# Optimization experiments

Measured on AMD Instinct MI355X. Metric: run time of the kernel, lower is better.

The kernel has to match this reference:

```python
import jax, jax.numpy as jnp
import numpy as np

DIM = 96
DIM_OUT = 96
NUM_HEADS = 1
HEAD_DIM = DIM_OUT // NUM_HEADS  # 96, also depthwise-conv channel count
STRIDE_Q = 1
STRIDE_KV = 2
EPS = 1e-6


def _layernorm(t, g, b):
    mu = jnp.mean(t, axis=-1, keepdims=True)
    var = jnp.mean(jnp.square(t - mu), axis=-1, keepdims=True)
    return (t - mu) * jax.lax.rsqrt(var + EPS) * g + b


def _depthwise(t_nchw, w, stride):
    # torch Conv2d(C, C, 3, stride, padding=1, groups=C, bias=False)
    # w: [C, 1, 3, 3]
    return jax.lax.conv_general_dilated(
        t_nchw, w, window_strides=(stride, stride), padding=[(1, 1), (1, 1)],
        feature_group_count=HEAD_DIM, dimension_numbers=('NCHW', 'OIHW', 'NCHW'))


def _attention_pool(t, w, stride, g, b, H, W):
    # t: [B, heads, L, C] -> pooled [B, heads, Lp, C]
    B, nh, L, C = t.shape
    t = t.reshape(B * nh, H, W, C).transpose(0, 3, 1, 2)  # [B*nh, C, H, W]
    t = _depthwise(t, w, stride)
    Hp, Wp = t.shape[2], t.shape[3]
    t = t.reshape(B, nh, C, Hp * Wp).transpose(0, 1, 3, 2)  # [B, nh, Lp, C]
    return _layernorm(t, g, b), Hp, Wp


def setup_inputs() -> dict:
    key = jax.random.key(0)
    ks = jax.random.split(key, 16)
    B, N = 32, 56 * 56
    inp = {
        'x': jax.random.normal(ks[0], (B, N, DIM), dtype=jnp.float32),
        'Wqkv': jax.random.normal(ks[1], (3 * DIM_OUT, DIM), dtype=jnp.float32) * 0.02,
        'bqkv': jax.random.normal(ks[2], (3 * DIM_OUT,), dtype=jnp.float32) * 0.02,
        'pool_q_w': jax.random.normal(ks[3], (HEAD_DIM, 1, 3, 3), dtype=jnp.float32) * 0.1,
        'gq': 1.0 + jax.random.normal(ks[4], (HEAD_DIM,), dtype=jnp.float32) * 0.02,
        'betq': jax.random.normal(ks[5], (HEAD_DIM,), dtype=jnp.float32) * 0.02,
        'pool_k_w': jax.random.normal(ks[6], (HEAD_DIM, 1, 3, 3), dtype=jnp.float32) * 0.1,
        'gk': 1.0 + jax.random.normal(ks[7], (HEAD_DIM,), dtype=jnp.float32) * 0.02,
        'betk': jax.random.normal(ks[8], (HEAD_DIM,), dtype=jnp.float32) * 0.02,
        'pool_v_w': jax.random.normal(ks[9], (HEAD_DIM, 1, 3, 3), dtype=jnp.float32) * 0.1,
        'gv': 1.0 + jax.random.normal(ks[10], (HEAD_DIM,), dtype=jnp.float32) * 0.02,
        'betv': jax.random.normal(ks[11], (HEAD_DIM,), dtype=jnp.float32) * 0.02,
        'Wproj': jax.random.normal(ks[12], (DIM_OUT, DIM_OUT), dtype=jnp.float32) * 0.02,
        'bproj': jax.random.normal(ks[13], (DIM_OUT,), dtype=jnp.float32) * 0.02,
        'h': 56,
        'w': 56,
    }
    return inp


def reference(x, Wqkv, bqkv, pool_q_w, gq, betq, pool_k_w, gk, betk,
              pool_v_w, gv, betv, Wproj, bproj, h, w):
    B, N, _ = x.shape
    qkv = (jnp.einsum('bnd,ed->bne', x, Wqkv) + bqkv)
    qkv = qkv.reshape(B, N, 3, NUM_HEADS, HEAD_DIM).transpose(2, 0, 3, 1, 4)
    q, k, v = qkv[0], qkv[1], qkv[2]  # each [B, heads, N, head_dim]

    q, Hq, Wq = _attention_pool(q, pool_q_w, STRIDE_Q, gq, betq, h, w)
    k, _, _ = _attention_pool(k, pool_k_w, STRIDE_KV, gk, betk, h, w)
    v, _, _ = _attention_pool(v, pool_v_w, STRIDE_KV, gv, betv, h, w)

    scale = HEAD_DIM ** -0.5
    attn = jax.nn.softmax(jnp.einsum('bhqc,bhkc->bhqk', q * scale, k), axis=-1)
    out = jnp.einsum('bhqk,bhkc->bhqc', attn, v) + q  # residual x + q
    out = out.transpose(0, 2, 1, 3).reshape(B, Hq * Wq, DIM_OUT)
    out = jnp.einsum('bnd,ed->bne', out, Wproj) + bproj
    return out
```

## Files before the change

kernel.cpp:

```cpp
#include <hip/hip_runtime.h>
#include <hip/hip_bf16.h>
#include <cmath>

#define BATCH 32
#define H_IN 56
#define W_IN 56
#define N_IN (H_IN * W_IN)
#define LKV 784
#define LKV_PAD 864
#define FRAG_ELEMS 82944

typedef short bf16x8 __attribute__((ext_vector_type(8)));
typedef float f32x4 __attribute__((ext_vector_type(4)));
typedef float f32x16 __attribute__((ext_vector_type(16)));

__device__ __forceinline__ unsigned pack_bf16(float a, float b) {
    unsigned ua = __builtin_bit_cast(unsigned, a);
    unsigned ub = __builtin_bit_cast(unsigned, b);
    ua = (ua + 0x7FFFu + ((ua >> 16) & 1u)) >> 16;
    ub = (ub + 0x7FFFu + ((ub >> 16) & 1u)) >> 16;
    return ua | (ub << 16);
}

__device__ __forceinline__ unsigned short cvt_bf16(float a) {
    unsigned ua = __builtin_bit_cast(unsigned, a);
    return (unsigned short)((ua + 0x7FFFu + ((ua >> 16) & 1u)) >> 16);
}

__device__ __forceinline__ float bf16_to_f32(unsigned short u) {
    unsigned v = ((unsigned)u) << 16;
    return __builtin_bit_cast(float, v);
}

__device__ __forceinline__ float bflo(unsigned u) {
    return __builtin_bit_cast(float, u << 16);
}
__device__ __forceinline__ float bfhi(unsigned u) {
    return __builtin_bit_cast(float, u & 0xFFFF0000u);
}

__device__ __forceinline__ unsigned pack_trunc(float a, float b) {
    return __builtin_amdgcn_perm(__builtin_bit_cast(unsigned, b),
                                 __builtin_bit_cast(unsigned, a), 0x07060302u);
}

__device__ __forceinline__ f32x16 zero16() {
    f32x16 z;
#pragma unroll
    for (int i = 0; i < 16; ++i) z[i] = 0.f;
    return z;
}

__global__ __launch_bounds__(256) void wprep_kernel(
    const float* __restrict__ Wqkv, const float* __restrict__ Wproj,
    const float* __restrict__ pqw, const float* __restrict__ pkw,
    const float* __restrict__ pvw,
    unsigned short* __restrict__ wq, unsigned short* __restrict__ wp,
    float* __restrict__ wpool)
{
    int idx = blockIdx.x * 256 + threadIdx.x;
    if (idx < 4608) {
        const float* src; unsigned short* dst; int li;
        if (idx < 3456) { src = Wqkv; dst = wq; li = idx; }
        else            { src = Wproj; dst = wp; li = idx - 3456; }
        int frag = li >> 6, ln = li & 63;
        int ct = frag / 3, kkb = frag % 3;
        int ch = ct * 16 + (ln & 15);
        int k0 = kkb * 32 + (ln >> 4) * 8;
        const float* s = src + ch * 96 + k0;
        float4 v0 = *reinterpret_cast<const float4*>(s);
        float4 v1 = *reinterpret_cast<const float4*>(s + 4);
        uint4 o;
        o.x = pack_bf16(v0.x, v0.y); o.y = pack_bf16(v0.z, v0.w);
        o.z = pack_bf16(v1.x, v1.y); o.w = pack_bf16(v1.z, v1.w);
        *reinterpret_cast<uint4*>(dst + (size_t)li * 8) = o;
    } else if (idx < 7200) {
        int li = idx - 4608;
        int which = li / 864, r = li % 864;
        int tap = r / 96, c = r % 96;
        const float* src = (which == 0) ? pqw : (which == 1 ? pkw : pvw);
        wpool[which * 864 + tap * 96 + c] = src[c * 9 + tap];
    }
}

template <int NCT, bool IN_BF16, bool OUT_F32>
__global__ __launch_bounds__(256, 2) void gemm2_kernel(
    const void* __restrict__ Xv, const unsigned short* __restrict__ Wfr,
    const float* __restrict__ bias, void* __restrict__ o0,
    void* __restrict__ o1, void* __restrict__ o2)
{
    __shared__ unsigned short Wl[NCT * 192 * 8];
    const int tid = threadIdx.x;
    const int wid = tid >> 6, lane = tid & 63;
    const int lo16 = lane & 15, hi = lane >> 4;

    for (int idx = tid; idx < NCT * 192; idx += 256)
        *reinterpret_cast<int4*>(&Wl[idx * 8]) =
            *reinterpret_cast<const int4*>(Wfr + (size_t)idx * 8);

    const size_t tok0 = (size_t)blockIdx.x * 256 + wid * 64;
    bf16x8 xb[12];
#pragma unroll
    for (int it = 0; it < 4; ++it) {
        size_t t = tok0 + it * 16 + lo16;
#pragma unroll
        for (int kkb = 0; kkb < 3; ++kkb) {
            if constexpr (IN_BF16) {
                xb[it * 3 + kkb] = *reinterpret_cast<const bf16x8*>(
                    (const unsigned short*)Xv + t * 96 + kkb * 32 + hi * 8);
            } else {
                const float* xp = (const float*)Xv + t * 96 + kkb * 32 + hi * 8;
                float4 a = *reinterpret_cast<const float4*>(xp);
                float4 c = *reinterpret_cast<const float4*>(xp + 4);
                uint4 u;
                u.x = pack_bf16(a.x, a.y); u.y = pack_bf16(a.z, a.w);
                u.z = pack_bf16(c.x, c.y); u.w = pack_bf16(c.z, c.w);
                xb[it * 3 + kkb] = __builtin_bit_cast(bf16x8, u);
            }
        }
    }
    __syncthreads();

#pragma unroll
    for (int ct = 0; ct < NCT; ++ct) {
        bf16x8 wf[3];
#pragma unroll
        for (int kkb = 0; kkb < 3; ++kkb)
            wf[kkb] = *reinterpret_cast<const bf16x8*>(&Wl[((ct * 3 + kkb) * 64 + lane) * 8]);
        const int chb = ct * 16 + hi * 4;
        float4 bv = *reinterpret_cast<const float4*>(bias + chb);
#pragma unroll
        for (int it = 0; it < 4; ++it) {
            f32x4 a = (f32x4){0.f, 0.f, 0.f, 0.f};
#pragma unroll
            for (int kkb = 0; kkb < 3; ++kkb)
                a = __builtin_amdgcn_mfma_f32_16x16x32_bf16(wf[kkb], xb[it * 3 + kkb], a, 0, 0, 0);
            size_t t = tok0 + it * 16 + lo16;
            float r0 = a[0] + bv.x, r1 = a[1] + bv.y;
            float r2 = a[2] + bv.z, r3 = a[3] + bv.w;
            if constexpr (OUT_F32) {
                *reinterpret_cast<float4*>((float*)o0 + t * 96 + chb) =
                    make_float4(r0, r1, r2, r3);
            } else {
                unsigned short* ob =
                    (unsigned short*)((ct < 6) ? o0 : (ct < 12 ? o1 : o2));
                int lch = (ct % 6) * 16 + hi * 4;
                uint2 p;
                p.x = pack_bf16(r0, r1);
                p.y = pack_bf16(r2, r3);
                *reinterpret_cast<uint2*>(ob + t * 96 + lch) = p;
            }
        }
    }
}

template <int OMODE, int STRIDE>
__global__ __launch_bounds__(192) void pool_ln4_kernel(
    const unsigned short* __restrict__ in, const float* __restrict__ pwt,
    const float* __restrict__ g, const float* __restrict__ beta,
    unsigned short* __restrict__ out, int Hp, int Wp, int LpPad, float oscale)
{
    __shared__ float2 part[192];
    __shared__ float2 mrs[16];
    const int tid = threadIdx.x;
    const int tok_l = tid / 12, c8 = tid % 12;
    const int gt = blockIdx.x * 16 + tok_l;
    const int Lp = Hp * Wp;
    const int b = gt / LpPad, rem = gt % LpPad;
    const bool pad = (rem >= Lp);
    const int yo = rem / Wp, xo = rem % Wp;

    float wt[9][8];
#pragma unroll
    for (int tap = 0; tap < 9; ++tap) {
        float4 w0 = *reinterpret_cast<const float4*>(pwt + tap * 96 + c8 * 8);
        float4 w1 = *reinterpret_cast<const float4*>(pwt + tap * 96 + c8 * 8 + 4);
        wt[tap][0] = w0.x; wt[tap][1] = w0.y; wt[tap][2] = w0.z; wt[tap][3] = w0.w;
        wt[tap][4] = w1.x; wt[tap][5] = w1.y; wt[tap][6] = w1.z; wt[tap][7] = w1.w;
    }

    float acc[8];
#pragma unroll
    for (int j = 0; j < 8; ++j) acc[j] = 0.f;

    const unsigned short* ib = in + (size_t)b * (H_IN * W_IN * 96) + c8 * 8;
#pragma unroll
    for (int dy = 0; dy < 3; ++dy) {
        const int iy = yo * STRIDE + dy - 1;
        if ((unsigned)iy < (unsigned)H_IN) {
#pragma unroll
            for (int dx = 0; dx < 3; ++dx) {
                const int ix = xo * STRIDE + dx - 1;
                if ((unsigned)ix < (unsigned)W_IN) {
                    const int tap = dy * 3 + dx;
                    uint4 d = *reinterpret_cast<const uint4*>(
                        ib + ((size_t)iy * W_IN + ix) * 96);
                    acc[0] += bflo(d.x) * wt[tap][0];
                    acc[1] += bfhi(d.x) * wt[tap][1];
                    acc[2] += bflo(d.y) * wt[tap][2];
                    acc[3] += bfhi(d.y) * wt[tap][3];
                    acc[4] += bflo(d.z) * wt[tap][4];
                    acc[5] += bfhi(d.z) * wt[tap][5];
                    acc[6] += bflo(d.w) * wt[tap][6];
                    acc[7] += bfhi(d.w) * wt[tap][7];
                }
            }
        }
    }

    float s = 0.f, s2 = 0.f;
#pragma unroll
    for (int j = 0; j < 8; ++j) { s += acc[j]; s2 += acc[j] * acc[j]; }
    part[tid] = make_float2(s, s2);
    __syncthreads();
    if (tid < 16) {
        float a = 0.f, q = 0.f;
#pragma unroll
        for (int j = 0; j < 12; ++j) {
            float2 p = part[tid * 12 + j];
            a += p.x; q += p.y;
        }
        float mu = a * (1.f / 96.f);
        float var = q * (1.f / 96.f) - mu * mu;
        mrs[tid] = make_float2(mu, rsqrtf(var + 1e-6f));
    }
    __syncthreads();
    const float mu = mrs[tok_l].x, rstd = mrs[tok_l].y;

    float4 g0 = *reinterpret_cast<const float4*>(g + c8 * 8);
    float4 g1 = *reinterpret_cast<const float4*>(g + c8 * 8 + 4);
    float4 b0 = *reinterpret_cast<const float4*>(beta + c8 * 8);
    float4 b1 = *reinterpret_cast<const float4*>(beta + c8 * 8 + 4);
    float r[8];
    r[0] = (acc[0] - mu) * rstd * (g0.x * oscale) + b0.x * oscale;
    r[1] = (acc[1] - mu) * rstd * (g0.y * oscale) + b0.y * oscale;
    r[2] = (acc[2] - mu) * rstd * (g0.z * oscale) + b0.z * oscale;
    r[3] = (acc[3] - mu) * rstd * (g0.w * oscale) + b0.w * oscale;
    r[4] = (acc[4] - mu) * rstd * (g1.x * oscale) + b1.x * oscale;
    r[5] = (acc[5] - mu) * rstd * (g1.y * oscale) + b1.y * oscale;
    r[6] = (acc[6] - mu) * rstd * (g1.z * oscale) + b1.z * oscale;
    r[7] = (acc[7] - mu) * rstd * (g1.w * oscale) + b1.w * oscale;
    if (OMODE != 0 && pad) {
#pragma unroll
        for (int j = 0; j < 8; ++j) r[j] = 0.f;
    }

    if constexpr (OMODE == 0) {
        uint4 o;
        o.x = pack_bf16(r[0], r[1]); o.y = pack_bf16(r[2], r[3]);
        o.z = pack_bf16(r[4], r[5]); o.w = pack_bf16(r[6], r[7]);
        *reinterpret_cast<uint4*>(out + (size_t)gt * 96 + c8 * 8) = o;
    } else if constexpr (OMODE == 1) {
        int t = rem >> 5, kkb = c8 >> 1, hi = c8 & 1;
        int ln = (rem & 31) | (hi << 5);
        uint4 o;
        o.x = pack_bf16(r[0], r[1]); o.y = pack_bf16(r[2], r[3]);
        o.z = pack_bf16(r[4], r[5]); o.w = pack_bf16(r[6], r[7]);
        *reinterpret_cast<uint4*>(out + (size_t)b * FRAG_ELEMS +
                                  ((size_t)(t * 6 + kkb) * 64 + ln) * 8) = o;
    } else {
        int kv16 = rem >> 4, e = rem & 7, lh = (rem >> 3) & 1;
#pragma unroll
        for (int j = 0; j < 8; ++j) {
            int j8 = c8 * 8 + j;
            int ct = j8 >> 5;
            int ln = (j8 & 31) | (lh << 5);
            out[(size_t)b * FRAG_ELEMS + ((size_t)(kv16 * 3 + ct) * 64 + ln) * 8 + e] =
                cvt_bf16(r[j]);
        }
    }
}

__global__ __launch_bounds__(64) void attn_mfma5_kernel(
    const unsigned short* __restrict__ qpl, const unsigned short* __restrict__ Kf,
    const unsigned short* __restrict__ Vf, unsigned short* __restrict__ out)
{
    const int bid = blockIdx.x;
    const int swz = (bid & 7) * 392 + (bid >> 3);
    const int b = swz / 98, qblk = swz % 98;
    const int lane = threadIdx.x;
    const int l31 = lane & 31, h = lane >> 5;

    const int qrow = qblk * 32 + l31;
    const unsigned short* qptr = qpl + ((size_t)b * N_IN + qrow) * 96;
    bf16x8 qf[6];
#pragma unroll
    for (int kkb = 0; kkb < 6; ++kkb)
        qf[kkb] = *reinterpret_cast<const bf16x8*>(qptr + kkb * 16 + h * 8);

    f32x16 a0 = zero16(), a1 = zero16(), a2 = zero16();
    float lsum = 0.f;

    const unsigned short* Kb = Kf + (size_t)b * FRAG_ELEMS;
    const unsigned short* Vb = Vf + (size_t)b * FRAG_ELEMS;

    for (int t = 0; t < 25; ++t) {
        bf16x8 kf[6];
#pragma unroll
        for (int kkb = 0; kkb < 6; ++kkb)
            kf[kkb] = *reinterpret_cast<const bf16x8*>(
                Kb + ((size_t)(t * 6 + kkb) * 64 + lane) * 8);

        __builtin_amdgcn_s_setprio(1);
        f32x16 s = zero16();
#pragma unroll
        for (int kkb = 0; kkb < 6; ++kkb)
            s = __builtin_amdgcn_mfma_f32_32x32x16_bf16(kf[kkb], qf[kkb], s, 0, 0, 0);
        __builtin_amdgcn_s_setprio(0);

        bf16x8 v0[3], v1[3];
#pragma unroll
        for (int ct = 0; ct < 3; ++ct) {
            v0[ct] = *reinterpret_cast<const bf16x8*>(
                Vb + ((size_t)((2 * t) * 3 + ct) * 64 + lane) * 8);
            v1[ct] = *reinterpret_cast<const bf16x8*>(
                Vb + ((size_t)((2 * t + 1) * 3 + ct) * 64 + lane) * 8);
        }

        const bool full = (t < 24);
        unsigned d[8], sw[8];
        {
            float p[16];
#pragma unroll
            for (int r = 0; r < 16; ++r) {
                float e = __builtin_amdgcn_exp2f(s[r]);
                p[r] = __builtin_bit_cast(float,
                         __builtin_bit_cast(unsigned, e) & 0xFFFF0000u);
            }
            float q0 = 0.f, q1 = 0.f;
#pragma unroll
            for (int r = 0; r < 8; ++r) { q0 += p[r]; q1 += p[r + 8]; }
            lsum += q0 + (full ? q1 : 0.f);
#pragma unroll
            for (int j = 0; j < 8; ++j) d[j] = pack_trunc(p[2 * j], p[2 * j + 1]);
        }
#pragma unroll
        for (int j = 0; j < 8; ++j)
            sw[j] = (unsigned)__shfl_xor((int)d[j], 32);

        {
            int4 bi = h ? make_int4((int)sw[2], (int)sw[3], (int)d[2], (int)d[3])
                        : make_int4((int)d[0], (int)d[1], (int)sw[0], (int)sw[1]);
            bf16x8 bf = __builtin_bit_cast(bf16x8, bi);
            __builtin_amdgcn_s_setprio(1);
            a0 = __builtin_amdgcn_mfma_f32_32x32x16_bf16(v0[0], bf, a0, 0, 0, 0);
            a1 = __builtin_amdgcn_mfma_f32_32x32x16_bf16(v0[1], bf, a1, 0, 0, 0);
            a2 = __builtin_amdgcn_mfma_f32_32x32x16_bf16(v0[2], bf, a2, 0, 0, 0);
            __builtin_amdgcn_s_setprio(0);
        }
        if (full) {
            int4 bi = h ? make_int4((int)sw[6], (int)sw[7], (int)d[6], (int)d[7])
                        : make_int4((int)d[4], (int)d[5], (int)sw[4], (int)sw[5]);
            bf16x8 bf = __builtin_bit_cast(bf16x8, bi);
            __builtin_amdgcn_s_setprio(1);
            a0 = __builtin_amdgcn_mfma_f32_32x32x16_bf16(v1[0], bf, a0, 0, 0, 0);
            a1 = __builtin_amdgcn_mfma_f32_32x32x16_bf16(v1[1], bf, a1, 0, 0, 0);
            a2 = __builtin_amdgcn_mfma_f32_32x32x16_bf16(v1[2], bf, a2, 0, 0, 0);
            __builtin_amdgcn_s_setprio(0);
        }
    }

    lsum += __shfl_xor(lsum, 32);
    const float inv = 1.f / lsum;

    unsigned short* op = out + ((size_t)b * N_IN + qrow) * 96;
#pragma unroll
    for (int ct = 0; ct < 3; ++ct) {
        const f32x16& a = (ct == 0) ? a0 : (ct == 1 ? a1 : a2);
#pragma unroll
        for (int gblk = 0; gblk < 4; ++gblk) {
            int ch = ct * 32 + gblk * 8 + 4 * h;
            ushort4 q4 = *reinterpret_cast<const ushort4*>(qptr + ch);
            uint2 pr;
            pr.x = pack_bf16(a[gblk * 4 + 0] * inv + bf16_to_f32(q4.x),
                             a[gblk * 4 + 1] * inv + bf16_to_f32(q4.y));
            pr.y = pack_bf16(a[gblk * 4 + 2] * inv + bf16_to_f32(q4.z),
                             a[gblk * 4 + 3] * inv + bf16_to_f32(q4.w));
            *reinterpret_cast<uint2*>(op + ch) = pr;
        }
    }
}

extern "C" void kernel_launch(void* const* d_in, const int* in_sizes, int n_in,
                              void* d_out, int out_size, void* d_ws, size_t ws_size,
                              hipStream_t stream)
{
    const float* x     = (const float*)d_in[0];
    const float* Wqkv  = (const float*)d_in[1];
    const float* bqkv  = (const float*)d_in[2];
    const float* pqw   = (const float*)d_in[3];
    const float* gq    = (const float*)d_in[4];
    const float* betq  = (const float*)d_in[5];
    const float* pkw   = (const float*)d_in[6];
    const float* gk    = (const float*)d_in[7];
    const float* betk  = (const float*)d_in[8];
    const float* pvw   = (const float*)d_in[9];
    const float* gv    = (const float*)d_in[10];
    const float* betv  = (const float*)d_in[11];
    const float* Wproj = (const float*)d_in[12];
    const float* bproj = (const float*)d_in[13];
    float* outp = (float*)d_out;

    char* ws = (char*)d_ws;
    const size_t QB    = (size_t)BATCH * N_IN * 96 * sizeof(short);
    const size_t FRAGB = (size_t)BATCH * FRAG_ELEMS * sizeof(short);
    unsigned short* qb   = (unsigned short*)(ws);
    unsigned short* kbuf = (unsigned short*)(ws + QB);
    unsigned short* vbuf = (unsigned short*)(ws + 2 * QB);
    unsigned short* qpb  = (unsigned short*)(ws + 3 * QB);
    unsigned short* Kfr  = (unsigned short*)(ws + 4 * QB);
    unsigned short* Vfr  = (unsigned short*)(ws + 4 * QB + FRAGB);
    unsigned short* wqf  = (unsigned short*)(ws + 4 * QB + 2 * FRAGB);
    unsigned short* wpf  = (unsigned short*)(ws + 4 * QB + 2 * FRAGB + 56320);
    float*          wpool = (float*)(ws + 4 * QB + 2 * FRAGB + 56320 + 18432);
    unsigned short* attn_out = qb;

    const int T = BATCH * N_IN;

    const float SC = 0.1020620726159658f * 1.4426950408889634f;

    wprep_kernel<<<29, 256, 0, stream>>>(Wqkv, Wproj, pqw, pkw, pvw, wqf, wpf, wpool);
    gemm2_kernel<18, false, false><<<T / 256, 256, 0, stream>>>(
        x, wqf, bqkv, qb, kbuf, vbuf);
    pool_ln4_kernel<0, 1><<<T / 16, 192, 0, stream>>>(
        qb, wpool, gq, betq, qpb, 56, 56, N_IN, 1.0f);
    pool_ln4_kernel<1, 2><<<(BATCH * LKV_PAD) / 16, 192, 0, stream>>>(
        kbuf, wpool + 864, gk, betk, Kfr, 28, 28, LKV_PAD, SC);
    pool_ln4_kernel<2, 2><<<(BATCH * LKV_PAD) / 16, 192, 0, stream>>>(
        vbuf, wpool + 1728, gv, betv, Vfr, 28, 28, LKV_PAD, 1.0f);
    attn_mfma5_kernel<<<3136, 64, 0, stream>>>(qpb, Kfr, Vfr, attn_out);
    gemm2_kernel<6, true, true><<<T / 256, 256, 0, stream>>>(
        attn_out, wpf, bproj, outp, nullptr, nullptr);
}
```

Before: 153.8 us.

## Split attention KV loop across four waves and reduce partials in LDS

The attention kernel now runs four wavefronts per 32-query block instead of one. The 25 KV tiles are strided across the waves, and each wave keeps its own output accumulators and row sum. Waves 1-3 write their partials to shared memory, and wave 0 adds them up, normalises and writes the result. The aim is to shorten the serial per-block loop and put more waves in flight to hide latency. The cost is about 37KB of LDS per block, a barrier, a reduction step, and uneven work across waves (7 versus 6 tiles).

```diff
diff --git a/kernel.cpp b/kernel.cpp
--- a/kernel.cpp
+++ b/kernel.cpp
@@ -271,14 +271,18 @@
     }
 }
 
-__global__ __launch_bounds__(64) void attn_mfma5_kernel(
+__global__ __launch_bounds__(256) void attn_mfma6_kernel(
     const unsigned short* __restrict__ qpl, const unsigned short* __restrict__ Kf,
     const unsigned short* __restrict__ Vf, unsigned short* __restrict__ out)
 {
+    __shared__ float partial[3][49][64];
+
     const int bid = blockIdx.x;
     const int swz = (bid & 7) * 392 + (bid >> 3);
     const int b = swz / 98, qblk = swz % 98;
-    const int lane = threadIdx.x;
+    const int tid = threadIdx.x;
+    const int wid = tid >> 6;
+    const int lane = tid & 63;
     const int l31 = lane & 31, h = lane >> 5;
 
     const int qrow = qblk * 32 + l31;
@@ -294,7 +298,7 @@
     const unsigned short* Kb = Kf + (size_t)b * FRAG_ELEMS;
     const unsigned short* Vb = Vf + (size_t)b * FRAG_ELEMS;
 
-    for (int t = 0; t < 25; ++t) {
+    for (int t = wid; t < 25; t += 4) {
         bf16x8 kf[6];
 #pragma unroll
         for (int kkb = 0; kkb < 6; ++kkb)
@@ -360,23 +364,48 @@
         }
     }
 
-    lsum += __shfl_xor(lsum, 32);
-    const float inv = 1.f / lsum;
-
-    unsigned short* op = out + ((size_t)b * N_IN + qrow) * 96;
-#pragma unroll
-    for (int ct = 0; ct < 3; ++ct) {
-        const f32x16& a = (ct == 0) ? a0 : (ct == 1 ? a1 : a2);
-#pragma unroll
-        for (int gblk = 0; gblk < 4; ++gblk) {
-            int ch = ct * 32 + gblk * 8 + 4 * h;
-            ushort4 q4 = *reinterpret_cast<const ushort4*>(qptr + ch);
-            uint2 pr;
-            pr.x = pack_bf16(a[gblk * 4 + 0] * inv + bf16_to_f32(q4.x),
-                             a[gblk * 4 + 1] * inv + bf16_to_f32(q4.y));
-            pr.y = pack_bf16(a[gblk * 4 + 2] * inv + bf16_to_f32(q4.z),
-                             a[gblk * 4 + 3] * inv + bf16_to_f32(q4.w));
-            *reinterpret_cast<uint2*>(op + ch) = pr;
+    if (wid != 0) {
+        float* dst = &partial[wid - 1][0][lane];
+#pragma unroll
+        for (int r = 0; r < 16; ++r) {
+            dst[r * 64]        = a0[r];
+            dst[(16 + r) * 64] = a1[r];
+            dst[(32 + r) * 64] = a2[r];
+        }
+        dst[48 * 64] = lsum;
+    }
+    __syncthreads();
+    if (wid == 0) {
+#pragma unroll
+        for (int w = 0; w < 3; ++w) {
+            const float* src = &partial[w][0][lane];
+#pragma unroll
+            for (int r = 0; r < 16; ++r) {
+                a0[r] += src[r * 64];
+                a1[r] += src[(16 + r) * 64];
+                a2[r] += src[(32 + r) * 64];
+            }
+            lsum += src[48 * 64];
+        }
+
+        lsum += __shfl_xor(lsum, 32);
+        const float inv = 1.f / lsum;
+
+        unsigned short* op = out + ((size_t)b * N_IN + qrow) * 96;
+#pragma unroll
+        for (int ct = 0; ct < 3; ++ct) {
+            const f32x16& a = (ct == 0) ? a0 : (ct == 1 ? a1 : a2);
+#pragma unroll
+            for (int gblk = 0; gblk < 4; ++gblk) {
+                int ch = ct * 32 + gblk * 8 + 4 * h;
+                ushort4 q4 = *reinterpret_cast<const ushort4*>(qptr + ch);
+                uint2 pr;
+                pr.x = pack_bf16(a[gblk * 4 + 0] * inv + bf16_to_f32(q4.x),
+                                 a[gblk * 4 + 1] * inv + bf16_to_f32(q4.y));
+                pr.y = pack_bf16(a[gblk * 4 + 2] * inv + bf16_to_f32(q4.z),
+                                 a[gblk * 4 + 3] * inv + bf16_to_f32(q4.w));
+                *reinterpret_cast<uint2*>(op + ch) = pr;
+            }
         }
     }
 }
@@ -428,7 +457,7 @@
         kbuf, wpool + 864, gk, betk, Kfr, 28, 28, LKV_PAD, SC);
     pool_ln4_kernel<2, 2><<<(BATCH * LKV_PAD) / 16, 192, 0, stream>>>(
         vbuf, wpool + 1728, gv, betv, Vfr, 28, 28, LKV_PAD, 1.0f);
-    attn_mfma5_kernel<<<3136, 64, 0, stream>>>(qpb, Kfr, Vfr, attn_out);
+    attn_mfma6_kernel<<<3136, 256, 0, stream>>>(qpb, Kfr, Vfr, attn_out);
     gemm2_kernel<6, true, true><<<T / 256, 256, 0, stream>>>(
         attn_out, wpf, bproj, outp, nullptr, nullptr);
 }
```

Result: slower. 192.9 us (+25.4%).
